# Performance work log

Hardware: AMD Instinct MI355X
Metric: run time of the kernel (lower is better)

## Reference

```python
import jax, jax.numpy as jnp
import numpy as np

B_, N, C = 4096, 49, 128
H = 4          # num_heads
NW = 64        # windows per image


def setup_inputs() -> dict:
    key = jax.random.key(0)
    k = jax.random.split(key, 6)
    s = 0.02
    return {
        "x": jax.random.normal(k[0], (B_, N, C), jnp.float32),
        "mask": jax.random.normal(k[1], (NW, N, N), jnp.float32),
        "qkv_w": jax.random.normal(k[2], (3 * C, C), jnp.float32) * s,
        "qkv_b": jax.random.normal(k[3], (3 * C,), jnp.float32) * s,
        "proj_w": jax.random.normal(k[4], (C, C), jnp.float32) * s,
        "proj_b": jax.random.normal(k[5], (C,), jnp.float32) * s,
    }


def reference(x, mask, qkv_w, qkv_b, proj_w, proj_b):
    b, n, c = x.shape
    hd = c // H
    scale = hd ** -0.5
    # fused QKV projection: [b, n, 3, H, hd] -> [3, b, H, n, hd]
    qkv = (x @ qkv_w.T + qkv_b).reshape(b, n, 3, H, hd)
    qkv = jnp.transpose(qkv, (2, 0, 3, 1, 4))
    q, k, v = qkv[0] * scale, qkv[1], qkv[2]
    attn = jnp.einsum("bhnd,bhmd->bhnm", q, k)  # [b, H, n, n]
    nW = mask.shape[0]
    attn = attn.reshape(b // nW, nW, H, n, n) + mask[None, :, None, :, :]
    attn = jax.nn.softmax(attn.reshape(b, H, n, n), axis=-1)
    out = jnp.einsum("bhnm,bhmd->bhnd", attn, v)
    out = jnp.transpose(out, (0, 2, 1, 3)).reshape(b, n, c)
    return out @ proj_w.T + proj_b
```

## Files before the change

### kernel.cpp

```cpp
#include <hip/hip_runtime.h>
#include <hip/hip_bf16.h>

#define C_DIM 128
#define HD 32
#define SCALE 0.17677669529663687f

typedef __attribute__((ext_vector_type(8))) short frag8;
typedef __attribute__((ext_vector_type(4))) float f32x4;

#define XBF_OFF 0
#define XBF_STR 136
#define MSK_OFF 8704
#define MSK_STR 52
#define HEAD_OFF 11264
#define HEAD_SZ 7424
#define Q_STR 40
#define VT_STR 72
#define P_STR 72
#define SMEM_TOT 40960

__device__ __forceinline__ unsigned short f2b(float x) {
    __hip_bfloat16 h = __float2bfloat16(x);
    return __builtin_bit_cast(unsigned short, h);
}
__device__ __forceinline__ float b2f(unsigned short u) {
    return __builtin_bit_cast(float, (unsigned)u << 16);
}

__global__ void convert_weights(const float4* __restrict__ qkvw,
                                const float4* __restrict__ projw,
                                ushort4* __restrict__ wbf) {
    int i = blockIdx.x * 256 + threadIdx.x;
    float4 v = (i < 12288) ? qkvw[i] : projw[i - 12288];
    ushort4 p;
    p.x = f2b(v.x); p.y = f2b(v.y); p.z = f2b(v.z); p.w = f2b(v.w);
    wbf[i] = p;
}

__global__ __launch_bounds__(512, 4) void attn_mfma(
    const float* __restrict__ x,
    const float* __restrict__ mask,
    const float* __restrict__ qkv_b,
    const float* __restrict__ proj_b,
    const unsigned short* __restrict__ wq,
    float* __restrict__ out)
{
    __shared__ __align__(16) unsigned short sm[SMEM_TOT];

    const int b = blockIdx.x, tid = threadIdx.x;
    const int wave = tid >> 6;
    const int h    = wave >> 1;
    const int half = wave & 1;
    const int lane = tid & 63;
    const int n16  = lane & 15;
    const int q    = lane >> 4;

    {
        const float4* xg = (const float4*)(x + (size_t)b * 6272);
        for (int i = tid; i < 1568; i += 512) {
            float4 v = xg[i];
            int row = i >> 5, col = (i & 31) << 2;
            ushort4 pk;
            pk.x = f2b(v.x); pk.y = f2b(v.y); pk.z = f2b(v.z); pk.w = f2b(v.w);
            *(ushort4*)&sm[XBF_OFF + row * XBF_STR + col] = pk;
        }
        for (int i = tid; i < 15 * XBF_STR; i += 512)
            sm[XBF_OFF + 49 * XBF_STR + i] = 0;
        const float* mg = mask + (size_t)(b & 63) * 2401;
        for (int i = tid; i < 2401; i += 512) {
            int r = i / 49, c = i - r * 49;
            sm[MSK_OFF + r * MSK_STR + c] = f2b(mg[i]);
        }
    }
    __syncthreads();

    const int Qb = HEAD_OFF + h * HEAD_SZ;
    const int Kb = Qb + 2560;
    const int Vb = Qb + 5120;
    const int Pb = Qb;

    frag8 a[2][4];
#pragma unroll
    for (int mt = 0; mt < 2; ++mt)
#pragma unroll
        for (int ks = 0; ks < 4; ++ks)
            a[mt][ks] = *(const frag8*)&sm[XBF_OFF + ((half * 2 + mt) * 16 + n16) * XBF_STR + ks * 32 + q * 8];

#pragma unroll
    for (int mat = 0; mat < 3; ++mat) {
#pragma unroll
        for (int nt = 0; nt < 2; ++nt) {
            const unsigned short* wrow = wq + (size_t)(mat * C_DIM + h * HD + nt * 16 + n16) * C_DIM;
            frag8 bf[4];
#pragma unroll
            for (int ks = 0; ks < 4; ++ks) bf[ks] = *(const frag8*)(wrow + ks * 32 + q * 8);
            float bias = qkv_b[mat * C_DIM + h * HD + nt * 16 + n16];
#pragma unroll
            for (int mt = 0; mt < 2; ++mt) {
                const int gm = half * 2 + mt;
                f32x4 acc = {0.f, 0.f, 0.f, 0.f};
#pragma unroll
                for (int ks = 0; ks < 4; ++ks)
                    acc = __builtin_amdgcn_mfma_f32_16x16x32_bf16(a[mt][ks], bf[ks], acc, 0, 0, 0);
                if (mat == 2) {
                    ushort4 pk;
                    pk.x = f2b(acc[0] + bias); pk.y = f2b(acc[1] + bias);
                    pk.z = f2b(acc[2] + bias); pk.w = f2b(acc[3] + bias);
                    *(ushort4*)&sm[Vb + (nt * 16 + n16) * VT_STR + gm * 16 + q * 4] = pk;
                } else {
                    const int base = (mat == 0) ? Qb : Kb;
                    const float sc = (mat == 0) ? SCALE : 1.f;
#pragma unroll
                    for (int r = 0; r < 4; ++r)
                        sm[base + (gm * 16 + q * 4 + r) * Q_STR + nt * 16 + n16] =
                            f2b((acc[r] + bias) * sc);
                }
            }
        }
    }
    __syncthreads();

    frag8 qf[2], kf[4];
#pragma unroll
    for (int mt = 0; mt < 2; ++mt)
        qf[mt] = *(const frag8*)&sm[Qb + ((half * 2 + mt) * 16 + n16) * Q_STR + q * 8];
#pragma unroll
    for (int t = 0; t < 4; ++t)
        kf[t] = *(const frag8*)&sm[Kb + (t * 16 + n16) * Q_STR + q * 8];

    f32x4 s[2][4];
#pragma unroll
    for (int mt = 0; mt < 2; ++mt)
#pragma unroll
        for (int nt = 0; nt < 4; ++nt) {
            int cc = min(nt * 16 + n16, 48);
#pragma unroll
            for (int r = 0; r < 4; ++r) {
                int rc = min((half * 2 + mt) * 16 + q * 4 + r, 48);
                s[mt][nt][r] = b2f(sm[MSK_OFF + rc * MSK_STR + cc]);
            }
            s[mt][nt] = __builtin_amdgcn_mfma_f32_16x16x32_bf16(qf[mt], kf[nt], s[mt][nt], 0, 0, 0);
        }

#pragma unroll
    for (int mt = 0; mt < 2; ++mt) {
#pragma unroll
        for (int r = 0; r < 4; ++r) {
            float mx = -1e30f;
#pragma unroll
            for (int nt = 0; nt < 4; ++nt)
                if (nt * 16 + n16 < 49) mx = fmaxf(mx, s[mt][nt][r]);
#pragma unroll
            for (int d = 1; d < 16; d <<= 1) mx = fmaxf(mx, __shfl_xor(mx, d));
            float sum = 0.f;
#pragma unroll
            for (int nt = 0; nt < 4; ++nt) {
                float e = (nt * 16 + n16 < 49) ? __expf(s[mt][nt][r] - mx) : 0.f;
                s[mt][nt][r] = e;
                sum += e;
            }
#pragma unroll
            for (int d = 1; d < 16; d <<= 1) sum += __shfl_xor(sum, d);
            float inv = __builtin_amdgcn_rcpf(sum);
#pragma unroll
            for (int nt = 0; nt < 4; ++nt) s[mt][nt][r] *= inv;
        }
    }
    __syncthreads();

#pragma unroll
    for (int mt = 0; mt < 2; ++mt)
#pragma unroll
        for (int nt = 0; nt < 4; ++nt)
#pragma unroll
            for (int r = 0; r < 4; ++r)
                sm[Pb + ((half * 2 + mt) * 16 + q * 4 + r) * P_STR + nt * 16 + n16] =
                    f2b(s[mt][nt][r]);

    frag8 vf[2][2];
#pragma unroll
    for (int nt = 0; nt < 2; ++nt)
#pragma unroll
        for (int ks = 0; ks < 2; ++ks)
            vf[nt][ks] = *(const frag8*)&sm[Vb + (nt * 16 + n16) * VT_STR + ks * 32 + q * 8];
    f32x4 o[2][2];
#pragma unroll
    for (int mt = 0; mt < 2; ++mt)
#pragma unroll
        for (int nt = 0; nt < 2; ++nt) o[mt][nt] = (f32x4){0.f, 0.f, 0.f, 0.f};
#pragma unroll
    for (int mt = 0; mt < 2; ++mt)
#pragma unroll
        for (int ks = 0; ks < 2; ++ks) {
            frag8 pf = *(const frag8*)&sm[Pb + ((half * 2 + mt) * 16 + n16) * P_STR + ks * 32 + q * 8];
#pragma unroll
            for (int nt = 0; nt < 2; ++nt)
                o[mt][nt] = __builtin_amdgcn_mfma_f32_16x16x32_bf16(pf, vf[nt][ks], o[mt][nt], 0, 0, 0);
        }

#pragma unroll
    for (int mt = 0; mt < 2; ++mt)
#pragma unroll
        for (int nt = 0; nt < 2; ++nt)
#pragma unroll
            for (int r = 0; r < 4; ++r)
                sm[XBF_OFF + ((half * 2 + mt) * 16 + q * 4 + r) * XBF_STR + h * HD + nt * 16 + n16] =
                    f2b(o[mt][nt][r]);
    __syncthreads();

    frag8 af[4][4];
#pragma unroll
    for (int mt = 0; mt < 4; ++mt)
#pragma unroll
        for (int ks = 0; ks < 4; ++ks)
            af[mt][ks] = *(const frag8*)&sm[XBF_OFF + (mt * 16 + n16) * XBF_STR + ks * 32 + q * 8];

    const unsigned short* pw = wq + 49152;
    float* outb = out + (size_t)b * 6272;
    {
        const unsigned short* wrow = pw + (size_t)(wave * 16 + n16) * C_DIM;
        frag8 bf[4];
#pragma unroll
        for (int ks = 0; ks < 4; ++ks) bf[ks] = *(const frag8*)(wrow + ks * 32 + q * 8);
        float bias = proj_b[wave * 16 + n16];
#pragma unroll
        for (int mt = 0; mt < 4; ++mt) {
            f32x4 acc = {0.f, 0.f, 0.f, 0.f};
#pragma unroll
            for (int ks = 0; ks < 4; ++ks)
                acc = __builtin_amdgcn_mfma_f32_16x16x32_bf16(af[mt][ks], bf[ks], acc, 0, 0, 0);
#pragma unroll
            for (int r = 0; r < 4; ++r) {
                int row = mt * 16 + q * 4 + r;
                if (row < 49) outb[row * C_DIM + wave * 16 + n16] = acc[r] + bias;
            }
        }
    }
}

extern "C" void kernel_launch(void* const* d_in, const int* in_sizes, int n_in,
                              void* d_out, int out_size, void* d_ws, size_t ws_size,
                              hipStream_t stream) {
    const float* x      = (const float*)d_in[0];
    const float* mask   = (const float*)d_in[1];
    const float* qkv_b  = (const float*)d_in[3];
    const float* proj_b = (const float*)d_in[5];

    unsigned short* wbf = (unsigned short*)d_ws;
    convert_weights<<<64, 256, 0, stream>>>((const float4*)d_in[2],
                                            (const float4*)d_in[4],
                                            (ushort4*)wbf);
    attn_mfma<<<4096, 512, 0, stream>>>(x, mask, qkv_b, proj_b, wbf, (float*)d_out);
}
```

Baseline: 294.3 us.

## Transpose MFMA operands for vectorized stores, read mask from global, shrink LDS

Swaps the A/B operands of several MFMAs so each lane's accumulator holds four consecutive output columns. Q, K, P and the output can then be stored as packed uint2 bf16 pairs to LDS and as float4 to global, instead of scalar stores. The mask is no longer staged in shared memory; it is read straight from global into the score accumulators. Head scratch now aliases the x buffer after an extra barrier, which cuts LDS use from 80KB to about 58KB per block and could raise occupancy, at the cost of more barriers and uncoalesced mask loads.

```diff
diff --git a/kernel.cpp b/kernel.cpp
--- a/kernel.cpp
+++ b/kernel.cpp
@@ -2,29 +2,24 @@
 #include <hip/hip_bf16.h>
 
 #define C_DIM 128
-#define HD 32
 #define SCALE 0.17677669529663687f
 
 typedef __attribute__((ext_vector_type(8))) short frag8;
 typedef __attribute__((ext_vector_type(4))) float f32x4;
 
-#define XBF_OFF 0
-#define XBF_STR 136
-#define MSK_OFF 8704
-#define MSK_STR 52
-#define HEAD_OFF 11264
 #define HEAD_SZ 7424
 #define Q_STR 40
 #define VT_STR 72
 #define P_STR 72
-#define SMEM_TOT 40960
+#define XBF_STR 136
+#define SMEM_TOT 29696
 
 __device__ __forceinline__ unsigned short f2b(float x) {
     __hip_bfloat16 h = __float2bfloat16(x);
     return __builtin_bit_cast(unsigned short, h);
 }
-__device__ __forceinline__ float b2f(unsigned short u) {
-    return __builtin_bit_cast(float, (unsigned)u << 16);
+__device__ __forceinline__ unsigned pk2(float a, float b) {
+    return ((unsigned)f2b(b) << 16) | (unsigned)f2b(a);
 }
 
 __global__ void convert_weights(const float4* __restrict__ qkvw,
@@ -60,60 +55,58 @@
         for (int i = tid; i < 1568; i += 512) {
             float4 v = xg[i];
             int row = i >> 5, col = (i & 31) << 2;
-            ushort4 pk;
-            pk.x = f2b(v.x); pk.y = f2b(v.y); pk.z = f2b(v.z); pk.w = f2b(v.w);
-            *(ushort4*)&sm[XBF_OFF + row * XBF_STR + col] = pk;
-        }
-        for (int i = tid; i < 15 * XBF_STR; i += 512)
-            sm[XBF_OFF + 49 * XBF_STR + i] = 0;
-        const float* mg = mask + (size_t)(b & 63) * 2401;
-        for (int i = tid; i < 2401; i += 512) {
-            int r = i / 49, c = i - r * 49;
-            sm[MSK_OFF + r * MSK_STR + c] = f2b(mg[i]);
-        }
-    }
-    __syncthreads();
-
-    const int Qb = HEAD_OFF + h * HEAD_SZ;
-    const int Kb = Qb + 2560;
-    const int Vb = Qb + 5120;
-    const int Pb = Qb;
-
-    frag8 a[2][4];
-#pragma unroll
-    for (int mt = 0; mt < 2; ++mt)
+            uint2 pk; pk.x = pk2(v.x, v.y); pk.y = pk2(v.z, v.w);
+            *(uint2*)&sm[row * XBF_STR + col] = pk;
+        }
+        if (tid < 510) *(ushort4*)&sm[49 * XBF_STR + tid * 4] = (ushort4){0, 0, 0, 0};
+    }
+    __syncthreads();
+
+    frag8 xf[2][4];
+#pragma unroll
+    for (int tt = 0; tt < 2; ++tt)
 #pragma unroll
         for (int ks = 0; ks < 4; ++ks)
-            a[mt][ks] = *(const frag8*)&sm[XBF_OFF + ((half * 2 + mt) * 16 + n16) * XBF_STR + ks * 32 + q * 8];
+            xf[tt][ks] = *(const frag8*)&sm[((half * 2 + tt) * 16 + n16) * XBF_STR + ks * 32 + q * 8];
+    __syncthreads();
+
+    const int Qb = h * HEAD_SZ, Kb = Qb + 2560, Vb = Qb + 5120, Pb = Qb;
 
 #pragma unroll
     for (int mat = 0; mat < 3; ++mat) {
 #pragma unroll
-        for (int nt = 0; nt < 2; ++nt) {
-            const unsigned short* wrow = wq + (size_t)(mat * C_DIM + h * HD + nt * 16 + n16) * C_DIM;
-            frag8 bf[4];
-#pragma unroll
-            for (int ks = 0; ks < 4; ++ks) bf[ks] = *(const frag8*)(wrow + ks * 32 + q * 8);
-            float bias = qkv_b[mat * C_DIM + h * HD + nt * 16 + n16];
-#pragma unroll
-            for (int mt = 0; mt < 2; ++mt) {
-                const int gm = half * 2 + mt;
-                f32x4 acc = {0.f, 0.f, 0.f, 0.f};
-#pragma unroll
-                for (int ks = 0; ks < 4; ++ks)
-                    acc = __builtin_amdgcn_mfma_f32_16x16x32_bf16(a[mt][ks], bf[ks], acc, 0, 0, 0);
-                if (mat == 2) {
-                    ushort4 pk;
-                    pk.x = f2b(acc[0] + bias); pk.y = f2b(acc[1] + bias);
-                    pk.z = f2b(acc[2] + bias); pk.w = f2b(acc[3] + bias);
-                    *(ushort4*)&sm[Vb + (nt * 16 + n16) * VT_STR + gm * 16 + q * 4] = pk;
-                } else {
-                    const int base = (mat == 0) ? Qb : Kb;
-                    const float sc = (mat == 0) ? SCALE : 1.f;
-#pragma unroll
-                    for (int r = 0; r < 4; ++r)
-                        sm[base + (gm * 16 + q * 4 + r) * Q_STR + nt * 16 + n16] =
-                            f2b((acc[r] + bias) * sc);
+        for (int ct = 0; ct < 2; ++ct) {
+            const unsigned short* wrow = wq + (size_t)(mat * C_DIM + h * 32 + ct * 16 + n16) * C_DIM;
+            frag8 wf[4];
+#pragma unroll
+            for (int ks = 0; ks < 4; ++ks) wf[ks] = *(const frag8*)(wrow + ks * 32 + q * 8);
+            if (mat < 2) {
+                float4 b4 = *(const float4*)(qkv_b + mat * C_DIM + h * 32 + ct * 16 + q * 4);
+                const float sc = (mat == 0) ? SCALE : 1.f;
+                const int base = (mat == 0) ? Qb : Kb;
+#pragma unroll
+                for (int tt = 0; tt < 2; ++tt) {
+                    f32x4 acc = {0.f, 0.f, 0.f, 0.f};
+#pragma unroll
+                    for (int ks = 0; ks < 4; ++ks)
+                        acc = __builtin_amdgcn_mfma_f32_16x16x32_bf16(wf[ks], xf[tt][ks], acc, 0, 0, 0);
+                    uint2 pk;
+                    pk.x = pk2((acc[0] + b4.x) * sc, (acc[1] + b4.y) * sc);
+                    pk.y = pk2((acc[2] + b4.z) * sc, (acc[3] + b4.w) * sc);
+                    *(uint2*)&sm[base + ((half * 2 + tt) * 16 + n16) * Q_STR + ct * 16 + q * 4] = pk;
+                }
+            } else {
+                float bias = qkv_b[2 * C_DIM + h * 32 + ct * 16 + n16];
+#pragma unroll
+                for (int tt = 0; tt < 2; ++tt) {
+                    f32x4 acc = {0.f, 0.f, 0.f, 0.f};
+#pragma unroll
+                    for (int ks = 0; ks < 4; ++ks)
+                        acc = __builtin_amdgcn_mfma_f32_16x16x32_bf16(xf[tt][ks], wf[ks], acc, 0, 0, 0);
+                    uint2 pk;
+                    pk.x = pk2(acc[0] + bias, acc[1] + bias);
+                    pk.y = pk2(acc[2] + bias, acc[3] + bias);
+                    *(uint2*)&sm[Vb + (ct * 16 + n16) * VT_STR + (half * 2 + tt) * 16 + q * 4] = pk;
                 }
             }
         }
@@ -122,119 +115,118 @@
 
     frag8 qf[2], kf[4];
 #pragma unroll
-    for (int mt = 0; mt < 2; ++mt)
-        qf[mt] = *(const frag8*)&sm[Qb + ((half * 2 + mt) * 16 + n16) * Q_STR + q * 8];
-#pragma unroll
-    for (int t = 0; t < 4; ++t)
-        kf[t] = *(const frag8*)&sm[Kb + (t * 16 + n16) * Q_STR + q * 8];
-
-    f32x4 s[2][4];
-#pragma unroll
-    for (int mt = 0; mt < 2; ++mt)
-#pragma unroll
-        for (int nt = 0; nt < 4; ++nt) {
-            int cc = min(nt * 16 + n16, 48);
+    for (int it = 0; it < 2; ++it)
+        qf[it] = *(const frag8*)&sm[Qb + ((half * 2 + it) * 16 + n16) * Q_STR + q * 8];
+#pragma unroll
+    for (int jt = 0; jt < 4; ++jt)
+        kf[jt] = *(const frag8*)&sm[Kb + (jt * 16 + n16) * Q_STR + q * 8];
+    __syncthreads();
+
+    const float* mrow = mask + (size_t)(b & 63) * 2401;
+    int ii[2];
+#pragma unroll
+    for (int it = 0; it < 2; ++it) ii[it] = min(half * 32 + it * 16 + n16, 48);
+
+    f32x4 s[4][2];
+#pragma unroll
+    for (int it = 0; it < 2; ++it) {
+#pragma unroll
+        for (int jt = 0; jt < 3; ++jt) {
+            const float* mp = mrow + ii[it] * 49 + jt * 16 + q * 4;
+            s[jt][it] = (f32x4){mp[0], mp[1], mp[2], mp[3]};
+        }
+        float m48 = (q == 0) ? mrow[ii[it] * 49 + 48] : 0.f;
+        s[3][it] = (f32x4){m48, 0.f, 0.f, 0.f};
+    }
+#pragma unroll
+    for (int jt = 0; jt < 4; ++jt)
+#pragma unroll
+        for (int it = 0; it < 2; ++it)
+            s[jt][it] = __builtin_amdgcn_mfma_f32_16x16x32_bf16(kf[jt], qf[it], s[jt][it], 0, 0, 0);
+
+#pragma unroll
+    for (int it = 0; it < 2; ++it) {
+        float mx = -1e30f;
+#pragma unroll
+        for (int jt = 0; jt < 4; ++jt)
+#pragma unroll
+            for (int r = 0; r < 4; ++r)
+                if (jt * 16 + q * 4 + r < 49) mx = fmaxf(mx, s[jt][it][r]);
+        mx = fmaxf(mx, __shfl_xor(mx, 16));
+        mx = fmaxf(mx, __shfl_xor(mx, 32));
+        float sum = 0.f;
+#pragma unroll
+        for (int jt = 0; jt < 4; ++jt)
 #pragma unroll
             for (int r = 0; r < 4; ++r) {
-                int rc = min((half * 2 + mt) * 16 + q * 4 + r, 48);
-                s[mt][nt][r] = b2f(sm[MSK_OFF + rc * MSK_STR + cc]);
-            }
-            s[mt][nt] = __builtin_amdgcn_mfma_f32_16x16x32_bf16(qf[mt], kf[nt], s[mt][nt], 0, 0, 0);
-        }
-
-#pragma unroll
-    for (int mt = 0; mt < 2; ++mt) {
-#pragma unroll
-        for (int r = 0; r < 4; ++r) {
-            float mx = -1e30f;
-#pragma unroll
-            for (int nt = 0; nt < 4; ++nt)
-                if (nt * 16 + n16 < 49) mx = fmaxf(mx, s[mt][nt][r]);
-#pragma unroll
-            for (int d = 1; d < 16; d <<= 1) mx = fmaxf(mx, __shfl_xor(mx, d));
-            float sum = 0.f;
-#pragma unroll
-            for (int nt = 0; nt < 4; ++nt) {
-                float e = (nt * 16 + n16 < 49) ? __expf(s[mt][nt][r] - mx) : 0.f;
-                s[mt][nt][r] = e;
+                float e = (jt * 16 + q * 4 + r < 49) ? __expf(s[jt][it][r] - mx) : 0.f;
+                s[jt][it][r] = e;
                 sum += e;
             }
-#pragma unroll
-            for (int d = 1; d < 16; d <<= 1) sum += __shfl_xor(sum, d);
-            float inv = __builtin_amdgcn_rcpf(sum);
-#pragma unroll
-            for (int nt = 0; nt < 4; ++nt) s[mt][nt][r] *= inv;
-        }
-    }
-    __syncthreads();
-
-#pragma unroll
-    for (int mt = 0; mt < 2; ++mt)
-#pragma unroll
-        for (int nt = 0; nt < 4; ++nt)
-#pragma unroll
-            for (int r = 0; r < 4; ++r)
-                sm[Pb + ((half * 2 + mt) * 16 + q * 4 + r) * P_STR + nt * 16 + n16] =
-                    f2b(s[mt][nt][r]);
+        sum += __shfl_xor(sum, 16);
+        sum += __shfl_xor(sum, 32);
+        float inv = __builtin_amdgcn_rcpf(sum);
+#pragma unroll
+        for (int jt = 0; jt < 4; ++jt) {
+            uint2 pk;
+            pk.x = pk2(s[jt][it][0] * inv, s[jt][it][1] * inv);
+            pk.y = pk2(s[jt][it][2] * inv, s[jt][it][3] * inv);
+            *(uint2*)&sm[Pb + (half * 32 + it * 16 + n16) * P_STR + jt * 16 + q * 4] = pk;
+        }
+    }
 
     frag8 vf[2][2];
 #pragma unroll
+    for (int ct = 0; ct < 2; ++ct)
+#pragma unroll
+        for (int ks = 0; ks < 2; ++ks)
+            vf[ct][ks] = *(const frag8*)&sm[Vb + (ct * 16 + n16) * VT_STR + ks * 32 + q * 8];
+    f32x4 o[2][2];
+#pragma unroll
+    for (int ct = 0; ct < 2; ++ct)
+#pragma unroll
+        for (int nt = 0; nt < 2; ++nt) o[ct][nt] = (f32x4){0.f, 0.f, 0.f, 0.f};
+#pragma unroll
     for (int nt = 0; nt < 2; ++nt)
 #pragma unroll
-        for (int ks = 0; ks < 2; ++ks)
-            vf[nt][ks] = *(const frag8*)&sm[Vb + (nt * 16 + n16) * VT_STR + ks * 32 + q * 8];
-    f32x4 o[2][2];
-#pragma unroll
-    for (int mt = 0; mt < 2; ++mt)
-#pragma unroll
-        for (int nt = 0; nt < 2; ++nt) o[mt][nt] = (f32x4){0.f, 0.f, 0.f, 0.f};
-#pragma unroll
-    for (int mt = 0; mt < 2; ++mt)
-#pragma unroll
         for (int ks = 0; ks < 2; ++ks) {
-            frag8 pf = *(const frag8*)&sm[Pb + ((half * 2 + mt) * 16 + n16) * P_STR + ks * 32 + q * 8];
-#pragma unroll
-            for (int nt = 0; nt < 2; ++nt)
-                o[mt][nt] = __builtin_amdgcn_mfma_f32_16x16x32_bf16(pf, vf[nt][ks], o[mt][nt], 0, 0, 0);
-        }
-
-#pragma unroll
-    for (int mt = 0; mt < 2; ++mt)
-#pragma unroll
-        for (int nt = 0; nt < 2; ++nt)
-#pragma unroll
-            for (int r = 0; r < 4; ++r)
-                sm[XBF_OFF + ((half * 2 + mt) * 16 + q * 4 + r) * XBF_STR + h * HD + nt * 16 + n16] =
-                    f2b(o[mt][nt][r]);
-    __syncthreads();
-
-    frag8 af[4][4];
-#pragma unroll
-    for (int mt = 0; mt < 4; ++mt)
-#pragma unroll
-        for (int ks = 0; ks < 4; ++ks)
-            af[mt][ks] = *(const frag8*)&sm[XBF_OFF + (mt * 16 + n16) * XBF_STR + ks * 32 + q * 8];
+            frag8 pf = *(const frag8*)&sm[Pb + ((half * 2 + nt) * 16 + n16) * P_STR + ks * 32 + q * 8];
+#pragma unroll
+            for (int ct = 0; ct < 2; ++ct)
+                o[ct][nt] = __builtin_amdgcn_mfma_f32_16x16x32_bf16(vf[ct][ks], pf, o[ct][nt], 0, 0, 0);
+        }
+    __syncthreads();
+
+#pragma unroll
+    for (int ct = 0; ct < 2; ++ct)
+#pragma unroll
+        for (int nt = 0; nt < 2; ++nt) {
+            uint2 pk;
+            pk.x = pk2(o[ct][nt][0], o[ct][nt][1]);
+            pk.y = pk2(o[ct][nt][2], o[ct][nt][3]);
+            *(uint2*)&sm[((half * 2 + nt) * 16 + n16) * XBF_STR + h * 32 + ct * 16 + q * 4] = pk;
+        }
+    __syncthreads();
 
     const unsigned short* pw = wq + 49152;
+    frag8 wf2[4];
+#pragma unroll
+    for (int ks = 0; ks < 4; ++ks)
+        wf2[ks] = *(const frag8*)(pw + (size_t)(wave * 16 + n16) * C_DIM + ks * 32 + q * 8);
+    float4 b4 = *(const float4*)(proj_b + wave * 16 + q * 4);
     float* outb = out + (size_t)b * 6272;
-    {
-        const unsigned short* wrow = pw + (size_t)(wave * 16 + n16) * C_DIM;
-        frag8 bf[4];
-#pragma unroll
-        for (int ks = 0; ks < 4; ++ks) bf[ks] = *(const frag8*)(wrow + ks * 32 + q * 8);
-        float bias = proj_b[wave * 16 + n16];
-#pragma unroll
-        for (int mt = 0; mt < 4; ++mt) {
-            f32x4 acc = {0.f, 0.f, 0.f, 0.f};
-#pragma unroll
-            for (int ks = 0; ks < 4; ++ks)
-                acc = __builtin_amdgcn_mfma_f32_16x16x32_bf16(af[mt][ks], bf[ks], acc, 0, 0, 0);
-#pragma unroll
-            for (int r = 0; r < 4; ++r) {
-                int row = mt * 16 + q * 4 + r;
-                if (row < 49) outb[row * C_DIM + wave * 16 + n16] = acc[r] + bias;
-            }
-        }
+#pragma unroll
+    for (int nt = 0; nt < 4; ++nt) {
+        f32x4 acc = {0.f, 0.f, 0.f, 0.f};
+#pragma unroll
+        for (int ks = 0; ks < 4; ++ks) {
+            frag8 af = *(const frag8*)&sm[(nt * 16 + n16) * XBF_STR + ks * 32 + q * 8];
+            acc = __builtin_amdgcn_mfma_f32_16x16x32_bf16(wf2[ks], af, acc, 0, 0, 0);
+        }
+        int tok = nt * 16 + n16;
+        if (tok < 49)
+            *(float4*)&outb[tok * C_DIM + wave * 16 + q * 4] =
+                make_float4(acc[0] + b4.x, acc[1] + b4.y, acc[2] + b4.z, acc[3] + b4.w);
     }
 }
 
```

Result: no change. 293.1 us (-0.4%).
